# Kernel tuning notes

Hardware: AMD Instinct MI355X
Metric: run time of the kernel (lower is better)

## Reference

```python
import jax, jax.numpy as jnp
import numpy as np
from jax import lax

B, S, E, H = 4, 1024, 512, 8
D = E // H


def setup_inputs() -> dict:
    key = jax.random.key(0)
    k1, k2, k3 = jax.random.split(key, 3)
    source = jax.random.normal(k1, (B, S, E), dtype=jnp.float32)
    target = jax.random.normal(k2, (B, S, E), dtype=jnp.float32)
    # orthogonal-initialized positional encoder [1, H, 1, D]; random rows are a fine stand-in
    enc = jax.random.normal(k3, (1, H, 1, D), dtype=jnp.float32)
    enc = enc / jnp.linalg.norm(enc, axis=-1, keepdims=True)
    return {
        "source": source,
        "target": target,
        "encoder": enc,
        "alpha": jnp.float32(1.0),
        "beta": jnp.float32(1.0),
        "gamma": jnp.float32(2.0),
    }


def _split_heads(x):
    b, s, e = x.shape
    return x.reshape(b, s, H, e // H).transpose(0, 2, 1, 3)  # [B,H,S,D]


def reference(source, target, encoder, alpha, beta, gamma):
    q = _split_heads(source)  # [B,H,S,D]
    k = _split_heads(target)  # [B,H,S,D]
    pe = encoder[0, :, 0, :]  # [H,D]

    # --- grammar (time) attention: sequential tanh recurrence over t ---
    def step(cc, k_t):
        # cc, k_t: [B,H,D]
        cc = jnp.tanh(cc * pe)
        out = jnp.einsum('bhsd,bhd->bhs', q, cc)  # [B,H,S]
        return k_t * cc, out  # decay_rate = 0.0

    cc0 = k[:, :, 0, :]                      # initial cumulative context
    k_ts = jnp.moveaxis(k, 2, 0)             # [S,B,H,D]
    _, outs = lax.scan(step, cc0, k_ts)      # outs: [S,B,H,S]
    grammar = jnp.moveaxis(outs, 0, 3) / jnp.sqrt(jnp.float32(D))  # [B,H,S,S]
    grammar = jax.nn.softmax(grammar, axis=-1)

    # --- semantic attention ---
    semantic = jnp.einsum('bhsd,bhtd->bhst', q, k) / 100.0  # [B,H,S,S]

    w = jax.nn.softmax((alpha * semantic + beta * grammar) / gamma, axis=-1)

    # merge_heads: [B,H,S,S] -> [B,S,H*S]
    wm = w.transpose(0, 2, 1, 3).reshape(B, S, H * S)
    # output: wm^T @ target -> [B, H*S, E]
    return jnp.matmul(wm.transpose(0, 2, 1), target)
```

## Files before the change

### kernel.cpp

```cpp
#include <hip/hip_runtime.h>
#include <hip/hip_bf16.h>
#include <stdint.h>

#define S_LEN 1024
#define E_DIM 512
#define H_NUM 8
#define D_DIM 64
#define B_NUM 4
#define BH_NUM 32

using s16x8 = __attribute__((ext_vector_type(8))) short;
using f32x4 = __attribute__((ext_vector_type(4))) float;
using us4   = __attribute__((ext_vector_type(4))) unsigned short;

typedef const __attribute__((address_space(1))) uint32_t gas_uint;
typedef __attribute__((address_space(3))) uint32_t las_uint;

static __device__ __forceinline__ unsigned short f2bf(float f) {
  __hip_bfloat16 h = __float2bfloat16(f);
  return __builtin_bit_cast(unsigned short, h);
}
static __device__ __forceinline__ float bf2f(unsigned short u) {
  return __bfloat162float(__builtin_bit_cast(__hip_bfloat16, u));
}

#define NB_RECUR 8
#define NB_PACK  2048
#define NB_TR    512

__global__ __launch_bounds__(256) void k_prep(const float* __restrict__ src,
                                              const float* __restrict__ tgt,
                                              const float* __restrict__ enc,
                                              __hip_bfloat16* __restrict__ qb,
                                              __hip_bfloat16* __restrict__ kb,
                                              __hip_bfloat16* __restrict__ cb,
                                              __hip_bfloat16* __restrict__ tT) {
  __shared__ float tile[64][65];
  const int bid = blockIdx.x;
  const int tid = threadIdx.x;

  if (bid < NB_RECUR) {
    int g = bid * 256 + tid;
    int d = g & 63;
    int bh = g >> 6;
    int h = bh & 7;
    int b = bh >> 3;
    float pe = enc[h * D_DIM + d];
    float pe2 = 2.0f * pe;
    const float* tp = tgt + (size_t)b * S_LEN * E_DIM + h * D_DIM + d;
    __hip_bfloat16* cp = cb + (size_t)bh * S_LEN * D_DIM + d;

    constexpr int CH = 32;
    float bufA[CH], bufB[CH];
#pragma unroll
    for (int i = 0; i < CH; ++i) bufA[i] = tp[(size_t)i * E_DIM];
    float cc = bufA[0];

#pragma unroll 1
    for (int ch = 0; ch < S_LEN / CH; ch += 2) {
      if (ch + 1 < S_LEN / CH) {
#pragma unroll
        for (int i = 0; i < CH; ++i)
          bufB[i] = tp[(size_t)((ch + 1) * CH + i) * E_DIM];
      }
#pragma unroll
      for (int i = 0; i < CH; ++i) {
        float m = cc * pe2;
        float e = __expf(-fabsf(m));
        float th = __builtin_copysignf((1.0f - e) * __builtin_amdgcn_rcpf(1.0f + e), m);
        cp[(size_t)(ch * CH + i) * D_DIM] = __float2bfloat16(th);
        cc = bufA[i] * th;
      }
      if (ch + 2 < S_LEN / CH) {
#pragma unroll
        for (int i = 0; i < CH; ++i)
          bufA[i] = tp[(size_t)((ch + 2) * CH + i) * E_DIM];
      }
#pragma unroll
      for (int i = 0; i < CH; ++i) {
        float m = cc * pe2;
        float e = __expf(-fabsf(m));
        float th = __builtin_copysignf((1.0f - e) * __builtin_amdgcn_rcpf(1.0f + e), m);
        cp[(size_t)((ch + 1) * CH + i) * D_DIM] = __float2bfloat16(th);
        cc = bufB[i] * th;
      }
    }
  } else if (bid < NB_RECUR + NB_PACK) {
    size_t i4 = ((size_t)(bid - NB_RECUR) * 256 + tid) * 4;
    float4 s4 = *reinterpret_cast<const float4*>(src + i4);
    float4 t4 = *reinterpret_cast<const float4*>(tgt + i4);
    int e = (int)(i4 & 511);
    size_t bs = i4 >> 9;
    int s = (int)(bs & 1023);
    int b = (int)(bs >> 10);
    int h = e >> 6, d = e & 63;
    size_t o = (((size_t)(b * H_NUM + h) * S_LEN) + s) * D_DIM + d;
    us4 qv = {f2bf(s4.x), f2bf(s4.y), f2bf(s4.z), f2bf(s4.w)};
    us4 kv = {f2bf(t4.x), f2bf(t4.y), f2bf(t4.z), f2bf(t4.w)};
    *reinterpret_cast<us4*>(qb + o) = qv;
    *reinterpret_cast<us4*>(kb + o) = kv;
  } else {
    int lb = bid - (NB_RECUR + NB_PACK);
    int sx = lb & 15, ey = (lb >> 4) & 7, b = lb >> 7;
    int e0 = ey * 64, s0 = sx * 64;
    int tx = tid & 63, ty = tid >> 6;
    const float* p = tgt + ((size_t)b * S_LEN + s0) * E_DIM + e0;
#pragma unroll
    for (int r = ty; r < 64; r += 4) tile[r][tx] = p[(size_t)r * E_DIM + tx];
    __syncthreads();
    __hip_bfloat16* q = tT + ((size_t)b * E_DIM + e0) * S_LEN + s0;
#pragma unroll
    for (int r = ty; r < 64; r += 4) q[(size_t)r * S_LEN + tx] = __float2bfloat16(tile[tx][r]);
  }
}

__global__ __launch_bounds__(256) void k_weights(const __hip_bfloat16* __restrict__ qb,
                                                 const __hip_bfloat16* __restrict__ kb,
                                                 const __hip_bfloat16* __restrict__ cb,
                                                 __hip_bfloat16* __restrict__ wt,
                                                 const float* __restrict__ pal,
                                                 const float* __restrict__ pbe,
                                                 const float* __restrict__ pga) {
  __shared__ unsigned short stage[4][3][2048];
  __shared__ float red0[4][16];
  __shared__ float red1[4][16];

  const int tid = threadIdx.x;
  const int wave = tid >> 6, lane = tid & 63;
  const int quad = lane >> 4, col = lane & 15;

  const int g = blockIdx.x;
  const int xcd = g & 7;
  const int r = g >> 3;
  const int bh = xcd * 4 + (r >> 6);
  const int s0 = (r & 63) * 16;

  const float alpha = pal[0], beta = pbe[0];
  const float inv_gamma = 1.0f / pga[0];
  const float sa = alpha * 0.01f * inv_gamma;
  const float sb = beta * inv_gamma;

  const __hip_bfloat16* qrow = qb + ((size_t)bh * S_LEN + s0 + col) * D_DIM;
  s16x8 a0 = *reinterpret_cast<const s16x8*>(qrow + quad * 8);
  s16x8 a1 = *reinterpret_cast<const s16x8*>(qrow + 32 + quad * 8);

  const int t_base = wave * 256;
  uint32_t stg[16][2];
  float    stk[16][4];

  const char* cbase = (const char*)(cb + ((size_t)bh * S_LEN + t_base) * D_DIM);
  const char* kbase = (const char*)(kb + ((size_t)bh * S_LEN + t_base) * D_DIM);
  const int so0 = ((lane >> 3) << 7) | (((lane & 7) ^ ((lane >> 3) & 7)) << 4);

  auto stage_it = [&](int it) {
    unsigned short* db = &stage[wave][it % 3][0];
    const char* cs = cbase + it * 2048;
    const char* ks = kbase + it * 2048;
    __builtin_amdgcn_global_load_lds((gas_uint*)(cs + so0),        (las_uint*)(db),        16, 0, 0);
    __builtin_amdgcn_global_load_lds((gas_uint*)(cs + so0 + 1024), (las_uint*)(db + 512),  16, 0, 0);
    __builtin_amdgcn_global_load_lds((gas_uint*)(ks + so0),        (las_uint*)(db + 1024), 16, 0, 0);
    __builtin_amdgcn_global_load_lds((gas_uint*)(ks + so0 + 1024), (las_uint*)(db + 1536), 16, 0, 0);
  };

  stage_it(0);
  stage_it(1);

  const int xswz = (col & 7) << 4;
  float lg[4] = {0.f, 0.f, 0.f, 0.f};
#pragma unroll
  for (int it = 0; it < 16; ++it) {
    if (it < 15) asm volatile("s_waitcnt vmcnt(4)" ::: "memory");
    else         asm volatile("s_waitcnt vmcnt(0)" ::: "memory");
    const char* cw = (const char*)&stage[wave][it % 3][0];
    const char* kw = cw + 2048;
    const int rb = col * 128;
    s16x8 cf0 = *reinterpret_cast<const s16x8*>(cw + rb + ((quad * 16) ^ xswz));
    s16x8 cf1 = *reinterpret_cast<const s16x8*>(cw + rb + ((64 + quad * 16) ^ xswz));
    s16x8 kf0 = *reinterpret_cast<const s16x8*>(kw + rb + ((quad * 16) ^ xswz));
    s16x8 kf1 = *reinterpret_cast<const s16x8*>(kw + rb + ((64 + quad * 16) ^ xswz));
    f32x4 dg = {0.f, 0.f, 0.f, 0.f};
    f32x4 dk = {0.f, 0.f, 0.f, 0.f};
    __builtin_amdgcn_s_setprio(1);
    dg = __builtin_amdgcn_mfma_f32_16x16x32_bf16(a0, cf0, dg, 0, 0, 0);
    dg = __builtin_amdgcn_mfma_f32_16x16x32_bf16(a1, cf1, dg, 0, 0, 0);
    dk = __builtin_amdgcn_mfma_f32_16x16x32_bf16(a0, kf0, dk, 0, 0, 0);
    dk = __builtin_amdgcn_mfma_f32_16x16x32_bf16(a1, kf1, dk, 0, 0, 0);
    __builtin_amdgcn_s_setprio(0);
    if (it + 2 < 16) stage_it(it + 2);
    uint32_t p0 = 0, p1 = 0;
#pragma unroll
    for (int i = 0; i < 4; ++i) {
      float gv = __expf(dg[i] * 0.125f);
      unsigned short u = f2bf(gv);
      lg[i] += bf2f(u);
      if (i < 2) p0 |= (uint32_t)u << (16 * i);
      else       p1 |= (uint32_t)u << (16 * (i - 2));
      stk[it][i] = dk[i];
    }
    stg[it][0] = p0;
    stg[it][1] = p1;
  }
#pragma unroll
  for (int m = 1; m < 16; m <<= 1) {
#pragma unroll
    for (int i = 0; i < 4; ++i) lg[i] += __shfl_xor(lg[i], m);
  }
  if (col == 0) {
#pragma unroll
    for (int i = 0; i < 4; ++i) red0[wave][quad * 4 + i] = lg[i];
  }
  __syncthreads();
  float ilg[4];
#pragma unroll
  for (int i = 0; i < 4; ++i) {
    int rr = quad * 4 + i;
    ilg[i] = 1.0f / (red0[0][rr] + red0[1][rr] + red0[2][rr] + red0[3][rr]);
  }

  float lw[4] = {0.f, 0.f, 0.f, 0.f};
#pragma unroll
  for (int it = 0; it < 16; ++it) {
#pragma unroll
    for (int i = 0; i < 4; ++i) {
      unsigned short u = (unsigned short)((i < 2 ? stg[it][0] >> (16 * i)
                                                 : stg[it][1] >> (16 * (i - 2))) & 0xffffu);
      float gv = bf2f(u) * ilg[i];
      float z = sa * stk[it][i] + sb * gv;
      float wv = __expf(z);
      stk[it][i] = wv;
      lw[i] += wv;
    }
  }
#pragma unroll
  for (int m = 1; m < 16; m <<= 1) {
#pragma unroll
    for (int i = 0; i < 4; ++i) lw[i] += __shfl_xor(lw[i], m);
  }
  if (col == 0) {
#pragma unroll
    for (int i = 0; i < 4; ++i) red1[wave][quad * 4 + i] = lw[i];
  }
  __syncthreads();
  float ilw[4];
#pragma unroll
  for (int i = 0; i < 4; ++i) {
    int rr = quad * 4 + i;
    ilw[i] = 1.0f / (red1[0][rr] + red1[1][rr] + red1[2][rr] + red1[3][rr]);
  }

  __hip_bfloat16* wrow = wt + ((size_t)bh * S_LEN + t_base + col) * S_LEN + s0 + quad * 4;
#pragma unroll
  for (int it = 0; it < 16; ++it) {
    us4 o;
#pragma unroll
    for (int i = 0; i < 4; ++i) o[i] = f2bf(stk[it][i] * ilw[i]);
    *reinterpret_cast<us4*>(wrow + (size_t)it * 16 * S_LEN) = o;
  }
}

__global__ __launch_bounds__(256) void k_outgemm(const __hip_bfloat16* __restrict__ wt,
                                                 const __hip_bfloat16* __restrict__ tT,
                                                 float* __restrict__ out) {
  __shared__ __hip_bfloat16 As[128 * 64];
  __shared__ __hip_bfloat16 Bs[128 * 64];
  const int tid = threadIdx.x;
  const int wave = tid >> 6, lane = tid & 63;
  const int quad = lane >> 4, col = lane & 15;

  const int g = blockIdx.x;
  const int xcd = g & 7;
  const int local = g >> 3;
  const int strip = xcd * 32 + (local >> 2);
  const int ntile = local & 3;
  const int bh = strip >> 3;
  const int mt = strip & 7;
  const int b = bh >> 3;
  const int m0 = mt * 128;
  const int n0 = ntile * 128;

  const __hip_bfloat16* Ag = wt + (size_t)bh * S_LEN * S_LEN;
  const __hip_bfloat16* Bg = tT + (size_t)b * E_DIM * S_LEN;
  const int mw = (wave >> 1) * 64, nw = (wave & 1) * 64;
  const int lrow = lane >> 3;
  const int lcol = (lane & 7) * 8;

  f32x4 acc[4][4];
#pragma unroll
  for (int i = 0; i < 4; ++i)
#pragma unroll
    for (int j = 0; j < 4; ++j) acc[i][j] = (f32x4){0.f, 0.f, 0.f, 0.f};

  for (int kt = 0; kt < 16; ++kt) {
    const int k0 = kt * 64;
    __syncthreads();
#pragma unroll
    for (int j = 0; j < 4; ++j) {
      int row = j * 32 + wave * 8 + lrow;
      const __hip_bfloat16* gp = Ag + (size_t)(m0 + row) * S_LEN + k0 + lcol;
      __builtin_amdgcn_global_load_lds((gas_uint*)gp,
                                       (las_uint*)(As + (j * 32 + wave * 8) * 64),
                                       16, 0, 0);
    }
#pragma unroll
    for (int j = 0; j < 4; ++j) {
      int row = j * 32 + wave * 8 + lrow;
      const __hip_bfloat16* gp = Bg + (size_t)(n0 + row) * S_LEN + k0 + lcol;
      __builtin_amdgcn_global_load_lds((gas_uint*)gp,
                                       (las_uint*)(Bs + (j * 32 + wave * 8) * 64),
                                       16, 0, 0);
    }
    __syncthreads();
#pragma unroll
    for (int ks = 0; ks < 2; ++ks) {
      s16x8 af[4], bf[4];
#pragma unroll
      for (int i = 0; i < 4; ++i)
        af[i] = *reinterpret_cast<const s16x8*>(As + (mw + i * 16 + col) * 64 + ks * 32 + quad * 8);
#pragma unroll
      for (int i = 0; i < 4; ++i)
        bf[i] = *reinterpret_cast<const s16x8*>(Bs + (nw + i * 16 + col) * 64 + ks * 32 + quad * 8);
#pragma unroll
      for (int mi = 0; mi < 4; ++mi)
#pragma unroll
        for (int ni = 0; ni < 4; ++ni)
          acc[mi][ni] = __builtin_amdgcn_mfma_f32_16x16x32_bf16(af[mi], bf[ni], acc[mi][ni], 0, 0, 0);
    }
  }

#pragma unroll
  for (int mi = 0; mi < 4; ++mi)
#pragma unroll
    for (int ni = 0; ni < 4; ++ni)
#pragma unroll
      for (int i = 0; i < 4; ++i) {
        int m = m0 + mw + mi * 16 + quad * 4 + i;
        int n = n0 + nw + ni * 16 + col;
        out[((size_t)bh * S_LEN + m) * E_DIM + n] = acc[mi][ni][i];
      }
}

extern "C" void kernel_launch(void* const* d_in, const int* in_sizes, int n_in,
                              void* d_out, int out_size, void* d_ws, size_t ws_size,
                              hipStream_t stream) {
  (void)in_sizes; (void)n_in; (void)out_size; (void)ws_size;
  const float* src = (const float*)d_in[0];
  const float* tgt = (const float*)d_in[1];
  const float* enc = (const float*)d_in[2];
  const float* pal = (const float*)d_in[3];
  const float* pbe = (const float*)d_in[4];
  const float* pga = (const float*)d_in[5];
  float* out = (float*)d_out;

  char* ws = (char*)d_ws;
  __hip_bfloat16* qb = (__hip_bfloat16*)(ws);
  __hip_bfloat16* kb = (__hip_bfloat16*)(ws + ((size_t)4 << 20));
  __hip_bfloat16* cb = (__hip_bfloat16*)(ws + ((size_t)8 << 20));
  __hip_bfloat16* tT = (__hip_bfloat16*)(ws + ((size_t)12 << 20));
  __hip_bfloat16* wt = (__hip_bfloat16*)(ws + ((size_t)16 << 20));

  k_prep<<<NB_RECUR + NB_PACK + NB_TR, 256, 0, stream>>>(src, tgt, enc, qb, kb, cb, tT);
  k_weights<<<dim3((S_LEN / 16) * BH_NUM), 256, 0, stream>>>(qb, kb, cb, wt, pal, pbe, pga);
  k_outgemm<<<dim3((E_DIM / 128) * (S_LEN / 128) * BH_NUM), 256, 0, stream>>>(wt, tT, out);
}
```

Baseline: 215.4 us.

## Double-buffer output GEMM LDS tiles with XOR swizzle and prefetch

The output GEMM now keeps two LDS buffers and issues the global-to-LDS loads for the next k-tile before computing the current one, using vmcnt waits and raw barriers instead of __syncthreads. The LDS layout is XOR-swizzled on the column chunk so the fragment reads avoid bank conflicts, and s_setprio raises wave priority around the MFMA section. The aim is to hide global load latency and cut LDS conflicts, at the cost of doubling LDS use per block, which may lower occupancy. It also depends on the hand-written vmcnt count being correct.

```diff
diff --git a/kernel.cpp b/kernel.cpp
--- a/kernel.cpp
+++ b/kernel.cpp
@@ -261,8 +261,8 @@
 __global__ __launch_bounds__(256) void k_outgemm(const __hip_bfloat16* __restrict__ wt,
                                                  const __hip_bfloat16* __restrict__ tT,
                                                  float* __restrict__ out) {
-  __shared__ __hip_bfloat16 As[128 * 64];
-  __shared__ __hip_bfloat16 Bs[128 * 64];
+  __shared__ __hip_bfloat16 As[2][128 * 64];
+  __shared__ __hip_bfloat16 Bs[2][128 * 64];
   const int tid = threadIdx.x;
   const int wave = tid >> 6, lane = tid & 63;
   const int quad = lane >> 4, col = lane & 15;
@@ -282,7 +282,7 @@
   const __hip_bfloat16* Bg = tT + (size_t)b * E_DIM * S_LEN;
   const int mw = (wave >> 1) * 64, nw = (wave & 1) * 64;
   const int lrow = lane >> 3;
-  const int lcol = (lane & 7) * 8;
+  const int lcolswz = ((lane & 7) ^ lrow) * 8;
 
   f32x4 acc[4][4];
 #pragma unroll
@@ -290,42 +290,58 @@
 #pragma unroll
     for (int j = 0; j < 4; ++j) acc[i][j] = (f32x4){0.f, 0.f, 0.f, 0.f};
 
-  for (int kt = 0; kt < 16; ++kt) {
+  auto stage = [&](int kt, int buf) {
     const int k0 = kt * 64;
-    __syncthreads();
 #pragma unroll
     for (int j = 0; j < 4; ++j) {
-      int row = j * 32 + wave * 8 + lrow;
-      const __hip_bfloat16* gp = Ag + (size_t)(m0 + row) * S_LEN + k0 + lcol;
-      __builtin_amdgcn_global_load_lds((gas_uint*)gp,
-                                       (las_uint*)(As + (j * 32 + wave * 8) * 64),
-                                       16, 0, 0);
-    }
-#pragma unroll
-    for (int j = 0; j < 4; ++j) {
-      int row = j * 32 + wave * 8 + lrow;
-      const __hip_bfloat16* gp = Bg + (size_t)(n0 + row) * S_LEN + k0 + lcol;
-      __builtin_amdgcn_global_load_lds((gas_uint*)gp,
-                                       (las_uint*)(Bs + (j * 32 + wave * 8) * 64),
-                                       16, 0, 0);
-    }
-    __syncthreads();
+      const int rbase = j * 32 + wave * 8;
+      const __hip_bfloat16* gpA = Ag + (size_t)(m0 + rbase + lrow) * S_LEN + k0 + lcolswz;
+      __builtin_amdgcn_global_load_lds((gas_uint*)gpA,
+                                       (las_uint*)(&As[buf][rbase * 64]), 16, 0, 0);
+      const __hip_bfloat16* gpB = Bg + (size_t)(n0 + rbase + lrow) * S_LEN + k0 + lcolswz;
+      __builtin_amdgcn_global_load_lds((gas_uint*)gpB,
+                                       (las_uint*)(&Bs[buf][rbase * 64]), 16, 0, 0);
+    }
+  };
+
+  const int swz = (col & 7) << 4;
+  auto compute = [&](int buf) {
+    const char* Ab = (const char*)&As[buf][0];
+    const char* Bb = (const char*)&Bs[buf][0];
+    __builtin_amdgcn_s_setprio(1);
 #pragma unroll
     for (int ks = 0; ks < 2; ++ks) {
-      s16x8 af[4], bf[4];
+      s16x8 af[4], bfr[4];
 #pragma unroll
       for (int i = 0; i < 4; ++i)
-        af[i] = *reinterpret_cast<const s16x8*>(As + (mw + i * 16 + col) * 64 + ks * 32 + quad * 8);
+        af[i] = *reinterpret_cast<const s16x8*>(
+            Ab + (size_t)(mw + i * 16 + col) * 128 + ((ks * 64 + quad * 16) ^ swz));
 #pragma unroll
       for (int i = 0; i < 4; ++i)
-        bf[i] = *reinterpret_cast<const s16x8*>(Bs + (nw + i * 16 + col) * 64 + ks * 32 + quad * 8);
+        bfr[i] = *reinterpret_cast<const s16x8*>(
+            Bb + (size_t)(nw + i * 16 + col) * 128 + ((ks * 64 + quad * 16) ^ swz));
 #pragma unroll
       for (int mi = 0; mi < 4; ++mi)
 #pragma unroll
         for (int ni = 0; ni < 4; ++ni)
-          acc[mi][ni] = __builtin_amdgcn_mfma_f32_16x16x32_bf16(af[mi], bf[ni], acc[mi][ni], 0, 0, 0);
-    }
-  }
+          acc[mi][ni] = __builtin_amdgcn_mfma_f32_16x16x32_bf16(af[mi], bfr[ni], acc[mi][ni], 0, 0, 0);
+    }
+    __builtin_amdgcn_s_setprio(0);
+  };
+
+  stage(0, 0);
+#pragma unroll 1
+  for (int kt = 0; kt < 15; ++kt) {
+    stage(kt + 1, (kt + 1) & 1);
+    asm volatile("s_waitcnt vmcnt(8)" ::: "memory");
+    __builtin_amdgcn_s_barrier();
+    compute(kt & 1);
+    asm volatile("" ::: "memory");
+    __builtin_amdgcn_s_barrier();
+  }
+  asm volatile("s_waitcnt vmcnt(0)" ::: "memory");
+  __builtin_amdgcn_s_barrier();
+  compute(1);
 
 #pragma unroll
   for (int mi = 0; mi < 4; ++mi)
```

Result: faster. 204.3 us (-5.2%).
